# Performance work log

Hardware: AMD Instinct MI355X
Metric: run time of the kernel (lower is better)

The kernel has to match this reference:

```python
import jax, jax.numpy as jnp
import numpy as np

L = 16384      # sequence length
D_IN = 512     # d_input
D_H = 1024     # d_hidden
D_OUT = 512    # d_output
R_MIN = 0.0
R_MAX = 0.99
MAX_PHASE = np.pi


def setup_inputs() -> dict:
    key = jax.random.key(0)
    k_nu, k_th, k_x, k_bre, k_bim, k_cre, k_cim, k_d = jax.random.split(key, 8)
    # nu_init with parametrization='exp'
    u_nu = jax.random.uniform(k_nu, (D_H,), dtype=jnp.float32)
    nu = jnp.sqrt(u_nu * (R_MAX ** 2 - R_MIN ** 2) + R_MIN ** 2)
    u_theta = jax.random.uniform(k_th, (D_H,), dtype=jnp.float32, minval=-MAX_PHASE, maxval=MAX_PHASE)
    theta = jnp.mod(u_theta, 2 * jnp.pi)
    lamb = jnp.stack([jnp.log(-jnp.log(nu)), jnp.log(theta)], axis=0)  # [2, D_H]
    # gamma_init with parametrization='exp': nu = exp(-exp(lamb[0]))
    nu_eff = jnp.exp(-jnp.exp(lamb[0]))
    gamma = jnp.log(jnp.sqrt(1.0 - jnp.abs(nu_eff) ** 2))  # [D_H]
    # matrix_init: normal / sqrt(shape[0])
    B_re = jax.random.normal(k_bre, (D_H, D_IN), dtype=jnp.float32) / jnp.sqrt(D_H)
    B_im = jax.random.normal(k_bim, (D_H, D_IN), dtype=jnp.float32) / jnp.sqrt(D_H)
    C_re = jax.random.normal(k_cre, (D_OUT, D_H), dtype=jnp.float32) / jnp.sqrt(D_OUT)
    C_im = jax.random.normal(k_cim, (D_OUT, D_H), dtype=jnp.float32) / jnp.sqrt(D_OUT)
    D = jax.random.normal(k_d, (D_OUT, D_IN), dtype=jnp.float32) / jnp.sqrt(D_OUT)
    inputs = jax.random.normal(k_x, (L, D_IN), dtype=jnp.float32)
    return {"inputs": inputs, "lamb": lamb, "gamma": gamma,
            "B_re": B_re, "B_im": B_im, "C_re": C_re, "C_im": C_im, "D": D}


def _binary_operator_diag(q_i, q_j):
    A_i, b_i = q_i
    A_j, b_j = q_j
    return (A_j * A_i, A_j * b_i + b_j)


def reference(inputs, lamb, gamma, B_re, B_im, C_re, C_im, D):
    # parametrization='exp': lambda = exp(-exp(nu_log) + i*exp(theta_log))
    diag_lambda = jnp.exp(-jnp.exp(lamb[0]) + 1j * jnp.exp(lamb[1]))  # [D_H] complex64
    # which_gamma='learned', exp param: scale rows of B by exp(gamma)
    B_norm = jnp.exp(gamma)[:, None] * (B_re + 1j * B_im)             # [D_H, D_IN]
    # Bu_t = B_norm @ x_t for all t, as one GEMM: [L, D_H] complex
    Bu = inputs.astype(B_norm.dtype) @ B_norm.T
    Lambda_elements = jnp.broadcast_to(diag_lambda[None, :], Bu.shape)
    # diagonal linear recurrence h_t = lambda*h_{t-1} + Bu_t via parallel scan
    _, h = jax.lax.associative_scan(_binary_operator_diag, (Lambda_elements, Bu))
    C = C_re + 1j * C_im
    # y_t = Re[C h_t] + D x_t
    outputs = jnp.real(h @ C.T) + inputs @ D.T  # [L, D_OUT]
    return outputs
```

## Files before the change

kernel.cpp:

```cpp
#include <hip/hip_runtime.h>

__device__ __forceinline__ unsigned short f2b(float f) {
    unsigned int u = __builtin_bit_cast(unsigned int, f);
    unsigned int r = (u + 0x7FFFu + ((u >> 16) & 1u)) >> 16;
    return (unsigned short)r;
}
__device__ __forceinline__ float b2f(unsigned short s) {
    unsigned int u = ((unsigned int)s) << 16;
    return __builtin_bit_cast(float, u);
}

typedef __attribute__((ext_vector_type(8))) short short8;
typedef __attribute__((ext_vector_type(4))) float float4v;

#define GLD16(g, l) __builtin_amdgcn_global_load_lds(                          \
    (const __attribute__((address_space(1))) unsigned int*)(g),                \
    (__attribute__((address_space(3))) unsigned int*)(l), 16, 0, 0)

#define SEQLEN 16384
#define NCHUNK 512
#define TCHUNK 32
#define LDH 2560

__global__ void prep_all(const float* __restrict__ x,
                         const float* __restrict__ B_re, const float* __restrict__ B_im,
                         const float* __restrict__ gamma,
                         const float* __restrict__ C_re, const float* __restrict__ C_im,
                         const float* __restrict__ Dm,
                         unsigned short* __restrict__ Hcat,
                         unsigned short* __restrict__ Bcat,
                         unsigned short* __restrict__ CW) {
    int b = blockIdx.x;
    if (b < 8192) {
        int id = b * 256 + threadIdx.x;
        int t = id >> 7;
        int k4 = (id & 127) << 2;
        float4 v = *(const float4*)(x + (long)t * 512 + k4);
        ushort4 o;
        o.x = f2b(v.x); o.y = f2b(v.y); o.z = f2b(v.z); o.w = f2b(v.w);
        *(ushort4*)(Hcat + (long)t * LDH + 2048 + k4) = o;
    } else if (b < 9216) {
        int id = (b - 8192) * 256 + threadIdx.x;
        int n = id >> 7;
        int k4 = (id & 127) << 2;
        const float* src = (n < 1024) ? (B_re + (long)n * 512) : (B_im + (long)(n - 1024) * 512);
        float g = expf(gamma[n & 1023]);
        float4 v = *(const float4*)(src + k4);
        ushort4 o;
        o.x = f2b(v.x * g); o.y = f2b(v.y * g); o.z = f2b(v.z * g); o.w = f2b(v.w * g);
        *(ushort4*)(Bcat + (long)n * 512 + k4) = o;
    } else {
        int id = (b - 9216) * 256 + threadIdx.x;
        int o = id / 640;
        int j4 = (id - o * 640) << 2;
        float4 v; float sgn = 1.0f;
        if (j4 < 1024) {
            v = *(const float4*)(C_re + (long)o * 1024 + j4);
        } else if (j4 < 2048) {
            v = *(const float4*)(C_im + (long)o * 1024 + (j4 - 1024));
            sgn = -1.0f;
        } else {
            v = *(const float4*)(Dm + (long)o * 512 + (j4 - 2048));
        }
        ushort4 w;
        w.x = f2b(v.x * sgn); w.y = f2b(v.y * sgn); w.z = f2b(v.z * sgn); w.w = f2b(v.w * sgn);
        *(ushort4*)(CW + (long)o * 2560 + j4) = w;
    }
}

template <bool OUT_BF16>
__launch_bounds__(256, 3)
__global__ void gemm_t128(const unsigned short* __restrict__ A, int lda,
                          const unsigned short* __restrict__ B, int ldb,
                          void* __restrict__ Cout, int ldc, int Ktot,
                          int nbx_shift) {
    __shared__ unsigned short sm[2][8192] __attribute__((aligned(16)));
    const int lane = threadIdx.x & 63;
    const int wid = threadIdx.x >> 6;

    const int bid = blockIdx.x;
    const int xcd = bid & 7;
    const int g = bid >> 3;
    const int bx = g & ((1 << nbx_shift) - 1);
    const int by = xcd * (gridDim.x >> (3 + nbx_shift)) + (g >> nbx_shift);
    const long m0 = (long)by * 128;
    const long n0 = (long)bx * 128;

    const int srow = lane >> 2;
    const int scol = (lane & 3) * 8;
    const unsigned short* Ag = A + (m0 + wid * 32 + srow) * (long)lda + scol;
    const unsigned short* Bg = B + (n0 + wid * 32 + srow) * (long)ldb + scol;

    const int fr = lane & 15;
    const int fk = (lane >> 4) * 8;
    const int wr = (wid >> 1) * 64;
    const int wc = (wid & 1) * 64;

    float4v acc[4][4] = {};
    short8 fa[4], fb[4];

    auto stage = [&](unsigned short* buf, int k0) {
        GLD16(Ag + k0, buf + wid * 1024);
        GLD16(Ag + (long)16 * lda + k0, buf + wid * 1024 + 512);
        GLD16(Bg + k0, buf + 4096 + wid * 1024);
        GLD16(Bg + (long)16 * ldb + k0, buf + 4096 + wid * 1024 + 512);
    };
    auto loadfrags = [&](const unsigned short* buf) {
#pragma unroll
        for (int i = 0; i < 4; i++)
            fa[i] = *(const short8*)(buf + (wr + i * 16 + fr) * 32 + fk);
#pragma unroll
        for (int j = 0; j < 4; j++)
            fb[j] = *(const short8*)(buf + 4096 + (wc + j * 16 + fr) * 32 + fk);
    };

    const int nk = Ktot >> 5;
    unsigned short* pc = sm[0];
    unsigned short* pn = sm[1];
    stage(pc, 0);
#pragma unroll 2
    for (int t = 0; t < nk; ++t) {
        __syncthreads();
        if (t + 1 < nk) stage(pn, (t + 1) * 32);
        loadfrags(pc);
#pragma unroll
        for (int mi = 0; mi < 4; mi++)
#pragma unroll
            for (int ni = 0; ni < 4; ni++)
                acc[mi][ni] = __builtin_amdgcn_mfma_f32_16x16x32_bf16(fa[mi], fb[ni], acc[mi][ni], 0, 0, 0);
        unsigned short* t2 = pc; pc = pn; pn = t2;
    }

    const int er = (lane >> 4) * 4;
    const int ec = lane & 15;
#pragma unroll
    for (int mi = 0; mi < 4; mi++) {
#pragma unroll
        for (int r = 0; r < 4; r++) {
            long grow = m0 + wr + mi * 16 + er + r;
#pragma unroll
            for (int ni = 0; ni < 4; ni++) {
                long gcol = n0 + wc + ni * 16 + ec;
                float v = acc[mi][ni][r];
                if (OUT_BF16)
                    ((unsigned short*)Cout)[grow * ldc + gcol] = f2b(v);
                else
                    ((float*)Cout)[grow * ldc + gcol] = v;
            }
        }
    }
}

__global__ void scan_ends(const unsigned short* __restrict__ Hcat,
                          const float* __restrict__ lamb,
                          float* __restrict__ E) {
    const int chunk = blockIdx.x;
    const int ch = threadIdx.x << 2;
    float lre[4], lim[4];
#pragma unroll
    for (int i = 0; i < 4; i++) {
        float nu = expf(-expf(lamb[ch + i]));
        float th = expf(lamb[1024 + ch + i]);
        lre[i] = nu * cosf(th);
        lim[i] = nu * sinf(th);
    }
    float hr[4] = {0, 0, 0, 0}, hi[4] = {0, 0, 0, 0};
    const unsigned short* base = Hcat + (long)chunk * TCHUNK * LDH + ch;
#pragma unroll 4
    for (int t = 0; t < TCHUNK; t++) {
        ushort4 br = *(const ushort4*)(base + (long)t * LDH);
        ushort4 bi = *(const ushort4*)(base + (long)t * LDH + 1024);
        float brf[4] = {b2f(br.x), b2f(br.y), b2f(br.z), b2f(br.w)};
        float bif[4] = {b2f(bi.x), b2f(bi.y), b2f(bi.z), b2f(bi.w)};
#pragma unroll
        for (int i = 0; i < 4; i++) {
            float nr = fmaf(lre[i], hr[i], fmaf(-lim[i], hi[i], brf[i]));
            float ni = fmaf(lre[i], hi[i], fmaf(lim[i], hr[i], bif[i]));
            hr[i] = nr; hi[i] = ni;
        }
    }
    float* Ec = E + (long)chunk * 2048 + ch;
#pragma unroll
    for (int i = 0; i < 4; i++) {
        Ec[i] = hr[i];
        Ec[1024 + i] = hi[i];
    }
}

__global__ void carry(const float* __restrict__ lamb, const float* __restrict__ E,
                      float* __restrict__ Kc) {
    const int ch = blockIdx.x * 256 + threadIdx.x;
    double nu = exp(-exp((double)lamb[ch]));
    double th = exp((double)lamb[1024 + ch]);
    double lr = nu * cos(th), li = nu * sin(th);
#pragma unroll
    for (int i = 0; i < 5; i++) {
        double rr = lr * lr - li * li;
        double ii = 2.0 * lr * li;
        lr = rr; li = ii;
    }
    float tre = (float)lr, tim = (float)li;
    float hr = 0.0f, hi = 0.0f;
#pragma unroll 8
    for (int c = 0; c < NCHUNK; c++) {
        Kc[(long)c * 2048 + ch] = hr;
        Kc[(long)c * 2048 + 1024 + ch] = hi;
        float er = E[(long)c * 2048 + ch];
        float ei = E[(long)c * 2048 + 1024 + ch];
        float nr = fmaf(tre, hr, fmaf(-tim, hi, er));
        float ni = fmaf(tre, hi, fmaf(tim, hr, ei));
        hr = nr; hi = ni;
    }
}

__global__ void scan_apply(unsigned short* __restrict__ Hcat,
                           const float* __restrict__ lamb,
                           const float* __restrict__ Kc) {
    const int chunk = blockIdx.x;
    const int ch = threadIdx.x << 2;
    float lre[4], lim[4];
#pragma unroll
    for (int i = 0; i < 4; i++) {
        float nu = expf(-expf(lamb[ch + i]));
        float th = expf(lamb[1024 + ch + i]);
        lre[i] = nu * cosf(th);
        lim[i] = nu * sinf(th);
    }
    float hr[4], hi[4];
#pragma unroll
    for (int i = 0; i < 4; i++) {
        hr[i] = Kc[(long)chunk * 2048 + ch + i];
        hi[i] = Kc[(long)chunk * 2048 + 1024 + ch + i];
    }
    unsigned short* base = Hcat + (long)chunk * TCHUNK * LDH + ch;
#pragma unroll 4
    for (int t = 0; t < TCHUNK; t++) {
        ushort4 br = *(const ushort4*)(base + (long)t * LDH);
        ushort4 bi = *(const ushort4*)(base + (long)t * LDH + 1024);
        float brf[4] = {b2f(br.x), b2f(br.y), b2f(br.z), b2f(br.w)};
        float bif[4] = {b2f(bi.x), b2f(bi.y), b2f(bi.z), b2f(bi.w)};
#pragma unroll
        for (int i = 0; i < 4; i++) {
            float nr = fmaf(lre[i], hr[i], fmaf(-lim[i], hi[i], brf[i]));
            float ni = fmaf(lre[i], hi[i], fmaf(lim[i], hr[i], bif[i]));
            hr[i] = nr; hi[i] = ni;
        }
        ushort4 orv, oiv;
        orv.x = f2b(hr[0]); orv.y = f2b(hr[1]); orv.z = f2b(hr[2]); orv.w = f2b(hr[3]);
        oiv.x = f2b(hi[0]); oiv.y = f2b(hi[1]); oiv.z = f2b(hi[2]); oiv.w = f2b(hi[3]);
        *(ushort4*)(base + (long)t * LDH) = orv;
        *(ushort4*)(base + (long)t * LDH + 1024) = oiv;
    }
}

extern "C" void kernel_launch(void* const* d_in, const int* in_sizes, int n_in,
                              void* d_out, int out_size, void* d_ws, size_t ws_size,
                              hipStream_t stream) {
    const float* x     = (const float*)d_in[0];
    const float* lamb  = (const float*)d_in[1];
    const float* gamma = (const float*)d_in[2];
    const float* B_re  = (const float*)d_in[3];
    const float* B_im  = (const float*)d_in[4];
    const float* C_re  = (const float*)d_in[5];
    const float* C_im  = (const float*)d_in[6];
    const float* Dm    = (const float*)d_in[7];

    char* ws = (char*)d_ws;
    unsigned short* Hcat = (unsigned short*)ws;
    float* E  = (float*)(ws + 83886080);
    float* Kc = E + (long)NCHUNK * 2048;
    unsigned short* Bcat = (unsigned short*)((char*)Kc + 4194304);
    unsigned short* CW   = Bcat + (long)2048 * 512;

    prep_all<<<10496, 256, 0, stream>>>(x, B_re, B_im, gamma, C_re, C_im, Dm, Hcat, Bcat, CW);
    gemm_t128<true><<<2048, 256, 0, stream>>>(Hcat + 2048, LDH, Bcat, 512, Hcat, LDH, 512,
                                              4);
    scan_ends<<<NCHUNK, 256, 0, stream>>>(Hcat, lamb, E);
    carry<<<4, 256, 0, stream>>>(lamb, E, Kc);
    scan_apply<<<NCHUNK, 256, 0, stream>>>(Hcat, lamb, Kc);
    gemm_t128<false><<<512, 256, 0, stream>>>(Hcat, LDH, CW, 2560, (float*)d_out, 512, 2560,
                                              2);
}
```

Before: 271.7 us.

## Replace GEMM with 8-wave ping-pong kernel, XOR-swizzled LDS and larger tiles

Replaces the 4-wave 128x128 bf16 GEMM with an 8-wave kernel whose tiles are 256 wide in N, with BM set by a template parameter (256 or 128). K-steps are 64 deep, and LDS rows are XOR-swizzled to avoid bank conflicts. The main loop is split into four MFMA quadrants separated by scheduling barriers, workgroup barriers and setprio. Global-to-LDS prefetch runs two stages ahead using explicit vmcnt waits. The aim is higher MFMA utilisation and better overlap of loads with compute in both GEMMs. The cost is fewer workgroups (512 and 256 blocks), which may under-fill 256 CUs and raise register pressure.

```diff
diff --git a/kernel.cpp b/kernel.cpp
--- a/kernel.cpp
+++ b/kernel.cpp
@@ -16,6 +16,10 @@
 #define GLD16(g, l) __builtin_amdgcn_global_load_lds(                          \
     (const __attribute__((address_space(1))) unsigned int*)(g),                \
     (__attribute__((address_space(3))) unsigned int*)(l), 16, 0, 0)
+
+#define WAIT_VMN(n) __builtin_amdgcn_s_waitcnt(0x0F70 | (n))
+#define SB()        __builtin_amdgcn_sched_barrier(0)
+#define BAR()       __builtin_amdgcn_s_barrier()
 
 #define SEQLEN 16384
 #define NCHUNK 512
@@ -68,80 +72,133 @@
     }
 }
 
-template <bool OUT_BF16>
-__launch_bounds__(256, 3)
-__global__ void gemm_t128(const unsigned short* __restrict__ A, int lda,
-                          const unsigned short* __restrict__ B, int ldb,
-                          void* __restrict__ Cout, int ldc, int Ktot,
-                          int nbx_shift) {
-    __shared__ unsigned short sm[2][8192] __attribute__((aligned(16)));
-    const int lane = threadIdx.x & 63;
-    const int wid = threadIdx.x >> 6;
+template <int MREP, bool OUT_BF16>
+__launch_bounds__(512, 2)
+__global__ void gemm_8p(const unsigned short* __restrict__ A, int lda,
+                        const unsigned short* __restrict__ B, int ldb,
+                        void* __restrict__ Cout, int ldc, int Ktot,
+                        int nbx_shift) {
+    constexpr int BM  = MREP * 32;
+    constexpr int ASH = BM * 64;
+    constexpr int NA  = BM / 64;
+    constexpr int GPT = NA + 4;
+    __shared__ unsigned short sm[2][ASH + 16384] __attribute__((aligned(16)));
+
+    const int tid  = threadIdx.x;
+    const int lane = tid & 63;
+    const int wid  = tid >> 6;
+    const int wr   = wid >> 2;
+    const int wc   = wid & 3;
 
     const int bid = blockIdx.x;
     const int xcd = bid & 7;
-    const int g = bid >> 3;
-    const int bx = g & ((1 << nbx_shift) - 1);
-    const int by = xcd * (gridDim.x >> (3 + nbx_shift)) + (g >> nbx_shift);
-    const long m0 = (long)by * 128;
-    const long n0 = (long)bx * 128;
-
-    const int srow = lane >> 2;
-    const int scol = (lane & 3) * 8;
-    const unsigned short* Ag = A + (m0 + wid * 32 + srow) * (long)lda + scol;
-    const unsigned short* Bg = B + (n0 + wid * 32 + srow) * (long)ldb + scol;
+    const int g   = bid >> 3;
+    const int bx  = g & ((1 << nbx_shift) - 1);
+    const int by  = xcd * (gridDim.x >> (3 + nbx_shift)) + (g >> nbx_shift);
+    const long m0 = (long)by * BM;
+    const long n0 = (long)bx * 256;
+
+    const int sr = lane >> 3;
+    const int sc = ((lane & 7) ^ sr) << 3;
+    const unsigned short* Agl = A + (m0 + sr) * (long)lda + sc;
+    const unsigned short* Bgl = B + (n0 + sr) * (long)ldb + sc;
 
     const int fr = lane & 15;
-    const int fk = (lane >> 4) * 8;
-    const int wr = (wid >> 1) * 64;
-    const int wc = (wid & 1) * 64;
-
-    float4v acc[4][4] = {};
-    short8 fa[4], fb[4];
-
-    auto stage = [&](unsigned short* buf, int k0) {
-        GLD16(Ag + k0, buf + wid * 1024);
-        GLD16(Ag + (long)16 * lda + k0, buf + wid * 1024 + 512);
-        GLD16(Bg + k0, buf + 4096 + wid * 1024);
-        GLD16(Bg + (long)16 * ldb + k0, buf + 4096 + wid * 1024 + 512);
-    };
-    auto loadfrags = [&](const unsigned short* buf) {
+    const int x7 = fr & 7;
+    const int k0off = (((lane >> 4)    ) ^ x7) << 3;
+    const int k1off = (((lane >> 4) + 4) ^ x7) << 3;
+
+    float4v acc[MREP][4] = {};
+    short8 fa[MREP / 2][2];
+    short8 fb[4][2];
+
+    auto stageB = [&](unsigned short* buf, long kt) {
+        unsigned short* ldsB = buf + ASH + wid * 512;
+        const unsigned short* gB = Bgl + kt;
 #pragma unroll
         for (int i = 0; i < 4; i++)
-            fa[i] = *(const short8*)(buf + (wr + i * 16 + fr) * 32 + fk);
-#pragma unroll
-        for (int j = 0; j < 4; j++)
-            fb[j] = *(const short8*)(buf + 4096 + (wc + j * 16 + fr) * 32 + fk);
-    };
-
-    const int nk = Ktot >> 5;
-    unsigned short* pc = sm[0];
-    unsigned short* pn = sm[1];
-    stage(pc, 0);
-#pragma unroll 2
+            GLD16(gB + (long)(8 * (wid + 8 * i)) * ldb, ldsB + i * 4096);
+    };
+    auto stageA = [&](unsigned short* buf, long kt) {
+        unsigned short* ldsA = buf + wid * 512;
+        const unsigned short* gA = Agl + kt;
+#pragma unroll
+        for (int i = 0; i < NA; i++)
+            GLD16(gA + (long)(8 * (wid + 8 * i)) * lda, ldsA + i * 4096);
+    };
+    auto ldA = [&](const unsigned short* buf, int mbase) {
+#pragma unroll
+        for (int i = 0; i < MREP / 2; i++) {
+            const unsigned short* p = buf + (wr * (BM / 2) + (mbase + i) * 16 + fr) * 64;
+            fa[i][0] = *(const short8*)(p + k0off);
+            fa[i][1] = *(const short8*)(p + k1off);
+        }
+    };
+    auto ldB = [&](const unsigned short* buf, int nbase) {
+#pragma unroll
+        for (int j = 0; j < 2; j++) {
+            const unsigned short* p = buf + ASH + (wc * 64 + (nbase + j) * 16 + fr) * 64;
+            fb[nbase + j][0] = *(const short8*)(p + k0off);
+            fb[nbase + j][1] = *(const short8*)(p + k1off);
+        }
+    };
+    auto mfmaQ = [&](int mbase, int nbase) {
+        __builtin_amdgcn_s_setprio(1);
+#pragma unroll
+        for (int i = 0; i < MREP / 2; i++)
+#pragma unroll
+            for (int j = 0; j < 2; j++) {
+                acc[mbase + i][nbase + j] = __builtin_amdgcn_mfma_f32_16x16x32_bf16(
+                    fa[i][0], fb[nbase + j][0], acc[mbase + i][nbase + j], 0, 0, 0);
+                acc[mbase + i][nbase + j] = __builtin_amdgcn_mfma_f32_16x16x32_bf16(
+                    fa[i][1], fb[nbase + j][1], acc[mbase + i][nbase + j], 0, 0, 0);
+            }
+        __builtin_amdgcn_s_setprio(0);
+    };
+
+    const int nk = Ktot >> 6;
+
+    stageB(sm[0], 0);  stageA(sm[0], 0);
+    stageB(sm[1], 64); stageA(sm[1], 64);
+    WAIT_VMN(GPT);
+    SB(); BAR(); SB();
+
     for (int t = 0; t < nk; ++t) {
-        __syncthreads();
-        if (t + 1 < nk) stage(pn, (t + 1) * 32);
-        loadfrags(pc);
-#pragma unroll
-        for (int mi = 0; mi < 4; mi++)
-#pragma unroll
-            for (int ni = 0; ni < 4; ni++)
-                acc[mi][ni] = __builtin_amdgcn_mfma_f32_16x16x32_bf16(fa[mi], fb[ni], acc[mi][ni], 0, 0, 0);
-        unsigned short* t2 = pc; pc = pn; pn = t2;
+        unsigned short* cur = sm[t & 1];
+        const bool st = (t + 2 < nk);
+        const long kt2 = (long)(t + 2) * 64;
+        ldA(cur, 0); ldB(cur, 0);
+        SB(); BAR(); SB();
+        mfmaQ(0, 0);
+        SB(); BAR(); SB();
+        ldB(cur, 2);
+        SB(); BAR(); SB();
+        mfmaQ(0, 2);
+        SB(); BAR(); SB();
+        if (st) stageB(cur, kt2);
+        ldA(cur, MREP / 2);
+        SB(); BAR(); SB();
+        mfmaQ(MREP / 2, 0);
+        SB(); BAR(); SB();
+        if (st) stageA(cur, kt2);
+        SB();
+        mfmaQ(MREP / 2, 2);
+        if (st)              WAIT_VMN(GPT);
+        else if (t + 1 < nk) WAIT_VMN(0);
+        SB(); BAR(); SB();
     }
 
     const int er = (lane >> 4) * 4;
     const int ec = lane & 15;
 #pragma unroll
-    for (int mi = 0; mi < 4; mi++) {
+    for (int mi = 0; mi < MREP; mi++) {
 #pragma unroll
         for (int r = 0; r < 4; r++) {
-            long grow = m0 + wr + mi * 16 + er + r;
-#pragma unroll
-            for (int ni = 0; ni < 4; ni++) {
-                long gcol = n0 + wc + ni * 16 + ec;
-                float v = acc[mi][ni][r];
+            long grow = m0 + wr * (BM / 2) + mi * 16 + er + r;
+#pragma unroll
+            for (int nj = 0; nj < 4; nj++) {
+                long gcol = n0 + wc * 64 + nj * 16 + ec;
+                float v = acc[mi][nj][r];
                 if (OUT_BF16)
                     ((unsigned short*)Cout)[grow * ldc + gcol] = f2b(v);
                 else
@@ -273,11 +330,11 @@
     unsigned short* CW   = Bcat + (long)2048 * 512;
 
     prep_all<<<10496, 256, 0, stream>>>(x, B_re, B_im, gamma, C_re, C_im, Dm, Hcat, Bcat, CW);
-    gemm_t128<true><<<2048, 256, 0, stream>>>(Hcat + 2048, LDH, Bcat, 512, Hcat, LDH, 512,
-                                              4);
+    gemm_8p<8, true><<<512, 512, 0, stream>>>(Hcat + 2048, LDH, Bcat, 512, Hcat, LDH, 512,
+                                              3);
     scan_ends<<<NCHUNK, 256, 0, stream>>>(Hcat, lamb, E);
     carry<<<4, 256, 0, stream>>>(lamb, E, Kc);
     scan_apply<<<NCHUNK, 256, 0, stream>>>(Hcat, lamb, Kc);
-    gemm_t128<false><<<512, 256, 0, stream>>>(Hcat, LDH, CW, 2560, (float*)d_out, 512, 2560,
-                                              2);
-}
+    gemm_8p<4, false><<<256, 512, 0, stream>>>(Hcat, LDH, CW, 2560, (float*)d_out, 512, 2560,
+                                               1);
+}
```

New measurement: 263.7 us. -2.9%, faster.
